# Kernel tuning notes

Hardware: AMD Instinct MI355X
Metric: run time of the kernel (lower is better)

Reference implementation:

```python
import jax, jax.numpy as jnp
import numpy as np

N, E = 50000, 800000
IN, EIN, HID, OUT = 128, 64, 256, 256
L, H = 3, 4
D = HID // H  # per-head out_feats


def setup_inputs() -> dict:
    key = jax.random.key(0)
    ks = jax.random.split(key, 20)
    s = 0.02
    return {
        "h": jax.random.normal(ks[0], (N, IN), jnp.float32),
        "efeat": jax.random.normal(ks[1], (E, EIN), jnp.float32),
        "src": jax.random.randint(ks[2], (E,), 0, N, jnp.int32),
        "dst": jax.random.randint(ks[3], (E,), 0, N, jnp.int32),
        "enc_w": jax.random.normal(ks[4], (IN, HID), jnp.float32) * s,
        "enc_b": jnp.zeros((HID,), jnp.float32),
        "eenc_w": jax.random.normal(ks[5], (EIN, HID), jnp.float32) * s,
        "eenc_b": jnp.zeros((HID,), jnp.float32),
        "Wn": jax.random.normal(ks[6], (L, HID, HID), jnp.float32) * s,
        "We": jax.random.normal(ks[7], (L, HID, HID), jnp.float32) * s,
        "al": jax.random.normal(ks[8], (L, H, D), jnp.float32) * s,
        "ar": jax.random.normal(ks[9], (L, H, D), jnp.float32) * s,
        "ae": jax.random.normal(ks[10], (L, H, D), jnp.float32) * s,
        "ln_g": jnp.ones((L, HID), jnp.float32),
        "ln_b": jnp.zeros((L, HID), jnp.float32),
        "out_w": jax.random.normal(ks[11], (HID, OUT), jnp.float32) * s,
        "out_b": jnp.zeros((OUT,), jnp.float32),
    }


def reference(h, efeat, src, dst, enc_w, enc_b, eenc_w, eenc_b,
              Wn, We, al, ar, ae, ln_g, ln_b, out_w, out_b):
    # Dropout layers act as identity (eval mode).
    n = h.shape[0]
    x = h @ enc_w + enc_b                      # [N, HID] node encoder
    ef = efeat @ eenc_w + eenc_b               # [E, HID] edge encoder
    nl, nh, nd = al.shape
    for l in range(nl):
        res = x
        feat = (x @ Wn[l]).reshape(n, nh, nd)          # [N,H,D]
        eft = (ef @ We[l]).reshape(-1, nh, nd)         # [E,H,D]
        el = jnp.sum(feat * al[l], axis=-1)            # [N,H]
        er = jnp.sum(feat * ar[l], axis=-1)            # [N,H]
        ee = jnp.sum(eft * ae[l], axis=-1)             # [E,H]
        e = jax.nn.leaky_relu(el[src] + er[dst] + ee, 0.2)  # [E,H]
        # edge softmax over incoming edges of each dst node
        m = jax.lax.stop_gradient(jax.ops.segment_max(e, dst, num_segments=n))
        a = jnp.exp(e - m[dst])
        ssum = jax.ops.segment_sum(a, dst, num_segments=n)
        alpha = a / ssum[dst]                          # [E,H]
        agg = jax.ops.segment_sum(alpha[:, :, None] * feat[src], dst,
                                  num_segments=n)      # [N,H,D]
        x = jax.nn.relu(agg.reshape(n, nh * nd))
        y = x + res
        mu = jnp.mean(y, axis=-1, keepdims=True)
        var = jnp.var(y, axis=-1, keepdims=True)
        x = (y - mu) / jnp.sqrt(var + 1e-5) * ln_g[l] + ln_b[l]
    return x @ out_w + out_b
```

## Files before the change

kernel.cpp:

```cpp
#include <hip/hip_runtime.h>
#include <math.h>


typedef __attribute__((ext_vector_type(8))) short bf16x8;
typedef __attribute__((ext_vector_type(8))) unsigned short u16x8;
typedef __attribute__((ext_vector_type(4))) float f32x4;

__device__ __forceinline__ ushort f2b(float f) {
    unsigned u; __builtin_memcpy(&u, &f, 4);
    unsigned r = u + 0x7FFF + ((u >> 16) & 1);
    return (ushort)(r >> 16);
}
__device__ __forceinline__ float b2f(ushort u) {
    unsigned x = (unsigned)u << 16;
    float f; __builtin_memcpy(&f, &x, 4);
    return f;
}

__global__ void k_deg(const int* __restrict__ dst, int* __restrict__ deg, int E) {
    int e = blockIdx.x * 256 + threadIdx.x;
    if (e < E) atomicAdd(&deg[dst[e]], 1);
}

__global__ void k_bsum(const int* __restrict__ deg, int* __restrict__ bsum, int n) {
    __shared__ int wsum[4];
    int tid = threadIdx.x;
    int idx = blockIdx.x * 1024 + tid * 4;
    int4 v = make_int4(0, 0, 0, 0);
    if (idx + 3 < n) v = *(const int4*)(deg + idx);
    else {
        if (idx + 0 < n) v.x = deg[idx + 0];
        if (idx + 1 < n) v.y = deg[idx + 1];
        if (idx + 2 < n) v.z = deg[idx + 2];
    }
    int s = v.x + v.y + v.z + v.w;
#pragma unroll
    for (int off = 32; off; off >>= 1) s += __shfl_down(s, off, 64);
    if ((tid & 63) == 0) wsum[tid >> 6] = s;
    __syncthreads();
    if (tid == 0) bsum[blockIdx.x] = wsum[0] + wsum[1] + wsum[2] + wsum[3];
}

__global__ void k_bscan(const int* __restrict__ bsum, int* __restrict__ boff,
                        int* __restrict__ rowp, int NB, int n) {
    int tid = threadIdx.x;
    int v = (tid < NB) ? bsum[tid] : 0;
    int sc = v;
#pragma unroll
    for (int off = 1; off < 64; off <<= 1) {
        int t = __shfl_up(sc, off, 64);
        if ((tid & 63) >= off) sc += t;
    }
    if (tid < NB) boff[tid] = sc - v;
    if (tid == 63) rowp[n] = sc;
}

__global__ void k_bwrite(const int* __restrict__ deg, const int* __restrict__ boff,
                         int* __restrict__ rowp, int* __restrict__ cursor, int n) {
    __shared__ int wsum[4];
    __shared__ int woff_sh[4];
    int tid = threadIdx.x;
    int lane = tid & 63, wid = tid >> 6;
    int idx = blockIdx.x * 1024 + tid * 4;
    int4 v = make_int4(0, 0, 0, 0);
    if (idx + 3 < n) v = *(const int4*)(deg + idx);
    else {
        if (idx + 0 < n) v.x = deg[idx + 0];
        if (idx + 1 < n) v.y = deg[idx + 1];
        if (idx + 2 < n) v.z = deg[idx + 2];
    }
    int sum4 = v.x + v.y + v.z + v.w;
    int sc = sum4;
#pragma unroll
    for (int off = 1; off < 64; off <<= 1) {
        int t = __shfl_up(sc, off, 64);
        if (lane >= off) sc += t;
    }
    if (lane == 63) wsum[wid] = sc;
    __syncthreads();
    if (tid < 4) {
        int o = 0;
        for (int w = 0; w < tid; w++) o += wsum[w];
        woff_sh[tid] = o;
    }
    __syncthreads();
    int ex = boff[blockIdx.x] + woff_sh[wid] + (sc - sum4);
    int p0 = ex, p1 = ex + v.x, p2 = p1 + v.y, p3 = p2 + v.z;
    if (idx + 0 < n) { rowp[idx + 0] = p0; cursor[idx + 0] = p0; }
    if (idx + 1 < n) { rowp[idx + 1] = p1; cursor[idx + 1] = p1; }
    if (idx + 2 < n) { rowp[idx + 2] = p2; cursor[idx + 2] = p2; }
    if (idx + 3 < n) { rowp[idx + 3] = p3; cursor[idx + 3] = p3; }
}

__global__ void k_scatter(const int* __restrict__ dst, const int* __restrict__ src,
                          int* __restrict__ cursor, int* __restrict__ eid,
                          int* __restrict__ esrc, int E) {
    int e = blockIdx.x * 256 + threadIdx.x;
    if (e < E) {
        int pos = atomicAdd(&cursor[dst[e]], 1);
        eid[pos] = e;
        esrc[pos] = src[e];
    }
}

__global__ void k_ew(const float* __restrict__ We, const float* __restrict__ ae,
                     float* __restrict__ ew) {
    int t = blockIdx.x * 256 + threadIdx.x;
    if (t >= 3072) return;
    int l = t >> 10, r = t & 1023;
    int k = r >> 2, h = r & 3;
    const float* w = We + (size_t)l * 65536 + (size_t)k * 256 + h * 64;
    const float* a = ae + l * 256 + h * 64;
    float s = 0.f;
    for (int d = 0; d < 64; d++) s += w[d] * a[d];
    ew[t] = s;
}

__global__ void k_eew(const float* __restrict__ eenc_w, const float* __restrict__ eenc_b,
                      const float* __restrict__ ew, float* __restrict__ eew2,
                      float* __restrict__ eeb) {
    int t = blockIdx.x * 256 + threadIdx.x;
    if (t < 768) {
        int j = t / 12, lh = t % 12;
        int l = lh >> 2, h = lh & 3;
        float s = 0.f;
        for (int k = 0; k < 256; k++) s += eenc_w[j * 256 + k] * ew[l * 1024 + k * 4 + h];
        eew2[j * 12 + lh] = s;
    } else if (t < 780) {
        int lh = t - 768;
        int l = lh >> 2, h = lh & 3;
        float s = 0.f;
        for (int k = 0; k < 256; k++) s += eenc_b[k] * ew[l * 1024 + k * 4 + h];
        eeb[lh] = s;
    }
}

__global__ __launch_bounds__(256) void k_ee(const float* __restrict__ efeat,
                                            const float* __restrict__ eew2,
                                            const float* __restrict__ eeb,
                                            const int* __restrict__ eid,
                                            float* __restrict__ ee_l,
                                            int E) {
    const int tid = threadIdx.x;
    const int lane = tid & 63;
    const int wave = tid >> 6;
    const int q = lane & 7;
    const int g8 = lane >> 3;

    float W[8][12];
#pragma unroll
    for (int u = 0; u < 4; u++)
#pragma unroll
        for (int t = 0; t < 12; t++) {
            W[u][t]     = eew2[(q * 4 + u) * 12 + t];
            W[u + 4][t] = eew2[(32 + q * 4 + u) * 12 + t];
        }
    float Bv[12];
#pragma unroll
    for (int t = 0; t < 12; t++) Bv[t] = eeb[t];

    const int base = blockIdx.x * 128 + wave * 32;
#pragma unroll
    for (int p = 0; p < 4; p++) {
        int pos = base + p * 8 + g8;
        if (pos >= E) return;
        int e = eid[pos];
        float4 v0 = *(const float4*)(efeat + (size_t)e * 64 + q * 4);
        float4 v1 = *(const float4*)(efeat + (size_t)e * 64 + 32 + q * 4);
        float acc[12];
#pragma unroll
        for (int t = 0; t < 12; t++)
            acc[t] = v0.x * W[0][t] + v0.y * W[1][t] + v0.z * W[2][t] + v0.w * W[3][t] +
                     v1.x * W[4][t] + v1.y * W[5][t] + v1.z * W[6][t] + v1.w * W[7][t];
#pragma unroll
        for (int m = 1; m < 8; m <<= 1)
#pragma unroll
            for (int t = 0; t < 12; t++) acc[t] += __shfl_xor(acc[t], m, 64);
        if (q == 0) {
#pragma unroll
            for (int l = 0; l < 3; l++) {
                float4 o = make_float4(acc[l * 4 + 0] + Bv[l * 4 + 0],
                                       acc[l * 4 + 1] + Bv[l * 4 + 1],
                                       acc[l * 4 + 2] + Bv[l * 4 + 2],
                                       acc[l * 4 + 3] + Bv[l * 4 + 3]);
                *(float4*)(ee_l + (size_t)l * E * 4 + (size_t)pos * 4) = o;
            }
        }
    }
}

__global__ void k_prep(const float* __restrict__ h, const float* __restrict__ enc_w,
                       const float* __restrict__ Wn, const float* __restrict__ out_w,
                       ushort* __restrict__ hb, ushort* __restrict__ encT,
                       ushort* __restrict__ WnT, ushort* __restrict__ outT, int n4) {
    int t = blockIdx.x * 256 + threadIdx.x;
    if (t < n4) {
        float4 v = *(const float4*)(h + (size_t)t * 4);
        ushort4 o;
        o.x = f2b(v.x); o.y = f2b(v.y); o.z = f2b(v.z); o.w = f2b(v.w);
        *(ushort4*)(hb + (size_t)t * 4) = o;
        return;
    }
    t -= n4;
    if (t < 32768) {
        int nn = t >> 7, k = t & 127;
        encT[t] = f2b(enc_w[k * 256 + nn]);
        return;
    }
    t -= 32768;
    if (t < 3 * 65536) {
        int l = t >> 16, r = t & 65535;
        int nn = r >> 8, k = r & 255;
        WnT[(size_t)l * 65536 + r] = f2b(Wn[(size_t)l * 65536 + k * 256 + nn]);
        return;
    }
    t -= 3 * 65536;
    if (t < 65536) {
        int nn = t >> 8, k = t & 255;
        outT[t] = f2b(out_w[k * 256 + nn]);
    }
}

template <int KTILES, bool BIAS, bool STORE_F32, bool STORE_BF16>
__global__ __launch_bounds__(256) void gemm_mfma(const ushort* __restrict__ A,
                                                 const ushort* __restrict__ BT,
                                                 const float* __restrict__ bias,
                                                 float* __restrict__ Cf,
                                                 ushort* __restrict__ Cb, int M) {
    constexpr int K = KTILES * 32;
    __shared__ __align__(16) ushort As[128 * 32];
    __shared__ __align__(16) ushort Bs[128 * 32];
    const int tid = threadIdx.x;
    const int wave = tid >> 6;
    const int lane = tid & 63;
    const int rowBase = blockIdx.x * 128;
    const int colBase = blockIdx.y * 128;
    const int sRow = lane >> 2;
    const int sCol = (lane & 3) * 8;
    const int c0 = wave * 2, c1 = wave * 2 + 1;

    const ushort* gA0 = A + (size_t)(rowBase + c0 * 16 + sRow) * K + sCol;
    const ushort* gA1 = A + (size_t)(rowBase + c1 * 16 + sRow) * K + sCol;
    const ushort* gB0 = BT + (size_t)(colBase + c0 * 16 + sRow) * K + sCol;
    const ushort* gB1 = BT + (size_t)(colBase + c1 * 16 + sRow) * K + sCol;
    ushort* lA0 = As + c0 * 512;
    ushort* lA1 = As + c1 * 512;
    ushort* lB0 = Bs + c0 * 512;
    ushort* lB1 = Bs + c1 * 512;

    f32x4 acc[4][4] = {};
    const int wr = (wave >> 1) * 64, wc = (wave & 1) * 64;
    const int ml = lane & 15, q = lane >> 4;

    for (int kt = 0; kt < KTILES; ++kt) {
        __builtin_amdgcn_global_load_lds(
            (const __attribute__((address_space(1))) unsigned*)(gA0 + kt * 32),
            (__attribute__((address_space(3))) unsigned*)lA0, 16, 0, 0);
        __builtin_amdgcn_global_load_lds(
            (const __attribute__((address_space(1))) unsigned*)(gA1 + kt * 32),
            (__attribute__((address_space(3))) unsigned*)lA1, 16, 0, 0);
        __builtin_amdgcn_global_load_lds(
            (const __attribute__((address_space(1))) unsigned*)(gB0 + kt * 32),
            (__attribute__((address_space(3))) unsigned*)lB0, 16, 0, 0);
        __builtin_amdgcn_global_load_lds(
            (const __attribute__((address_space(1))) unsigned*)(gB1 + kt * 32),
            (__attribute__((address_space(3))) unsigned*)lB1, 16, 0, 0);
        __syncthreads();
        bf16x8 af[4], bfr[4];
#pragma unroll
        for (int i = 0; i < 4; i++)
            af[i] = *(const bf16x8*)&As[(wr + i * 16 + ml) * 32 + q * 8];
#pragma unroll
        for (int j = 0; j < 4; j++)
            bfr[j] = *(const bf16x8*)&Bs[(wc + j * 16 + ml) * 32 + q * 8];
#pragma unroll
        for (int i = 0; i < 4; i++)
#pragma unroll
            for (int j = 0; j < 4; j++)
                acc[i][j] = __builtin_amdgcn_mfma_f32_16x16x32_bf16(af[i], bfr[j], acc[i][j],
                                                                    0, 0, 0);
        __syncthreads();
    }

#pragma unroll
    for (int j = 0; j < 4; j++) {
        const int col = colBase + wc + j * 16 + ml;
        const float bb = BIAS ? bias[col] : 0.f;
#pragma unroll
        for (int i = 0; i < 4; i++) {
#pragma unroll
            for (int r = 0; r < 4; r++) {
                const int row = rowBase + wr + i * 16 + q * 4 + r;
                if (row < M) {
                    float v = acc[i][j][r] + bb;
                    if (STORE_F32) Cf[(size_t)row * 256 + col] = v;
                    if (STORE_BF16) Cb[(size_t)row * 256 + col] = f2b(v);
                }
            }
        }
    }
}

__global__ __launch_bounds__(256) void k_elr(const ushort* __restrict__ feat,
                                             const float* __restrict__ al,
                                             const float* __restrict__ ar,
                                             float* __restrict__ el,
                                             float* __restrict__ er, int N) {
    int lane = threadIdx.x & 63;
    int n = blockIdx.x * 4 + (threadIdx.x >> 6);
    if (n >= N) return;
    ushort4 f4 = *(const ushort4*)&feat[(size_t)n * 256 + lane * 4];
    float4 a4 = *(const float4*)&al[lane * 4];
    float4 r4 = *(const float4*)&ar[lane * 4];
    float f0 = b2f(f4.x), f1 = b2f(f4.y), f2 = b2f(f4.z), f3 = b2f(f4.w);
    float va = f0 * a4.x + f1 * a4.y + f2 * a4.z + f3 * a4.w;
    float vr = f0 * r4.x + f1 * r4.y + f2 * r4.z + f3 * r4.w;
#pragma unroll
    for (int m = 1; m < 16; m <<= 1) {
        va += __shfl_xor(va, m, 64);
        vr += __shfl_xor(vr, m, 64);
    }
    if ((lane & 15) == 0) {
        int h = lane >> 4;
        el[n * 4 + h] = va;
        er[n * 4 + h] = vr;
    }
}

__global__ __launch_bounds__(256) void k_agg(const int* __restrict__ rowp,
                                             const int* __restrict__ esrc,
                                             const float* __restrict__ ee,
                                             const float* __restrict__ el,
                                             const float* __restrict__ er,
                                             const ushort* __restrict__ feat,
                                             ushort* __restrict__ xb,
                                             const float* __restrict__ g,
                                             const float* __restrict__ b, int N) {
    __shared__ float w_sh[4][64][4];
    __shared__ int s_sh[4][64];
    const int wv = threadIdx.x >> 6;
    const int lane = threadIdx.x & 63;
    const int n = blockIdx.x * 4 + wv;
    if (n >= N) return;
    const int start = rowp[n], end = rowp[n + 1];
    const int half = lane >> 5;
    const int c = lane & 31;
    const int h = c >> 3;

    float4 e4 = *(const float4*)(er + (size_t)n * 4);
    float ern[4] = {e4.x, e4.y, e4.z, e4.w};
    float wsum[4] = {0.f, 0.f, 0.f, 0.f};
    float acc[8] = {0.f, 0.f, 0.f, 0.f, 0.f, 0.f, 0.f, 0.f};

    for (int cs = start; cs < end; cs += 64) {
        const int m = min(64, end - cs);
        if (lane < m) {
            int pos = cs + lane;
            int s = esrc[pos];
            s_sh[wv][lane] = s;
            float4 eev = *(const float4*)(ee + (size_t)pos * 4);
            float4 elv = *(const float4*)(el + (size_t)s * 4);
            float ea[4] = {eev.x, eev.y, eev.z, eev.w};
            float la[4] = {elv.x, elv.y, elv.z, elv.w};
#pragma unroll
            for (int hh = 0; hh < 4; hh++) {
                float sc = la[hh] + ern[hh] + ea[hh];
                sc = (sc > 0.f) ? sc : 0.2f * sc;
                float w = __expf(sc);
                w_sh[wv][lane][hh] = w;
                wsum[hh] += w;
            }
        }
        asm volatile("s_waitcnt lgkmcnt(0)" ::: "memory");
        __builtin_amdgcn_sched_barrier(0);
        for (int j = half; j < m; j += 2) {
            int s = s_sh[wv][j];
            float w = w_sh[wv][j][h];
            u16x8 p = *(const u16x8*)&feat[(size_t)s * 256 + c * 8];
#pragma unroll
            for (int u = 0; u < 8; u++) acc[u] += w * b2f((ushort)p[u]);
        }
        asm volatile("s_waitcnt lgkmcnt(0)" ::: "memory");
        __builtin_amdgcn_sched_barrier(0);
    }

#pragma unroll
    for (int u = 0; u < 8; u++) acc[u] += __shfl_xor(acc[u], 32, 64);

#pragma unroll
    for (int mm = 1; mm < 64; mm <<= 1)
#pragma unroll
        for (int hh = 0; hh < 4; hh++) wsum[hh] += __shfl_xor(wsum[hh], mm, 64);

    float inv = (end > start) ? 1.f / wsum[h] : 0.f;
    u16x8 xr = *(const u16x8*)&xb[(size_t)n * 256 + c * 8];
    float y[8];
    float s1 = 0.f, s2 = 0.f;
#pragma unroll
    for (int u = 0; u < 8; u++) {
        float v = fmaxf(acc[u] * inv, 0.f);
        y[u] = v + b2f((ushort)xr[u]);
        s1 += y[u];
        s2 += y[u] * y[u];
    }
#pragma unroll
    for (int mm = 1; mm < 64; mm <<= 1) {
        s1 += __shfl_xor(s1, mm, 64);
        s2 += __shfl_xor(s2, mm, 64);
    }
    float mu = s1 * (1.f / 512.f);
    float var = s2 * (1.f / 512.f) - mu * mu;
    float rstd = rsqrtf(var + 1e-5f);
    float4 gv0 = *(const float4*)&g[c * 8];
    float4 gv1 = *(const float4*)&g[c * 8 + 4];
    float4 bv0 = *(const float4*)&b[c * 8];
    float4 bv1 = *(const float4*)&b[c * 8 + 4];
    float ga[8] = {gv0.x, gv0.y, gv0.z, gv0.w, gv1.x, gv1.y, gv1.z, gv1.w};
    float ba[8] = {bv0.x, bv0.y, bv0.z, bv0.w, bv1.x, bv1.y, bv1.z, bv1.w};
    u16x8 ob;
#pragma unroll
    for (int u = 0; u < 8; u++) ob[u] = f2b((y[u] - mu) * rstd * ga[u] + ba[u]);
    if (half == 0)
        *(u16x8*)&xb[(size_t)n * 256 + c * 8] = ob;
}

extern "C" void kernel_launch(void* const* d_in, const int* in_sizes, int n_in,
                              void* d_out, int out_size, void* d_ws, size_t ws_size,
                              hipStream_t stream) {
    const float* h      = (const float*)d_in[0];
    const float* efeat  = (const float*)d_in[1];
    const int*   src    = (const int*)d_in[2];
    const int*   dst    = (const int*)d_in[3];
    const float* enc_w  = (const float*)d_in[4];
    const float* enc_b  = (const float*)d_in[5];
    const float* eenc_w = (const float*)d_in[6];
    const float* eenc_b = (const float*)d_in[7];
    const float* Wn     = (const float*)d_in[8];
    const float* We     = (const float*)d_in[9];
    const float* al     = (const float*)d_in[10];
    const float* ar     = (const float*)d_in[11];
    const float* ae     = (const float*)d_in[12];
    const float* ln_g   = (const float*)d_in[13];
    const float* ln_b   = (const float*)d_in[14];
    const float* out_w  = (const float*)d_in[15];
    const float* out_b  = (const float*)d_in[16];

    const int N = in_sizes[0] / 128;
    const int E = in_sizes[2];
    const int Mpad = ((N + 127) / 128) * 128;
    const int NB = (N + 1023) / 1024;

    char* ws = (char*)d_ws;
    size_t off = 0;
    auto alloc = [&](size_t bytes) -> char* {
        char* p = ws + off;
        off += (bytes + 255) & ~(size_t)255;
        return p;
    };
    ushort* Xb     = (ushort*)alloc((size_t)Mpad * 256 * 2);
    ushort* F      = (ushort*)alloc((size_t)Mpad * 256 * 2);
    ushort* hb     = (ushort*)alloc((size_t)Mpad * 128 * 2);
    float*  el     = (float*)alloc((size_t)N * 4 * 4);
    float*  er     = (float*)alloc((size_t)N * 4 * 4);
    float*  ee_l   = (float*)alloc((size_t)E * 12 * 4);
    int*    esrc   = (int*)alloc((size_t)E * 4);
    int*    eid    = (int*)alloc((size_t)E * 4);
    int*    deg    = (int*)alloc((size_t)N * 4);
    int*    rowp   = (int*)alloc((size_t)(N + 1) * 4);
    int*    cursor = (int*)alloc((size_t)N * 4);
    int*    bsum   = (int*)alloc(64 * 4);
    int*    boff   = (int*)alloc(64 * 4);
    float*  ew     = (float*)alloc(3072 * 4);
    float*  eew2   = (float*)alloc(768 * 4);
    float*  eeb    = (float*)alloc(64);
    ushort* encT   = (ushort*)alloc(256 * 128 * 2);
    ushort* WnT    = (ushort*)alloc(3 * 256 * 256 * 2);
    ushort* outT   = (ushort*)alloc(256 * 256 * 2);
    (void)ws_size; (void)n_in; (void)out_size;

    hipMemsetAsync(deg, 0, (size_t)N * 4, stream);
    k_deg<<<(E + 255) / 256, 256, 0, stream>>>(dst, deg, E);
    k_bsum<<<NB, 256, 0, stream>>>(deg, bsum, N);
    k_bscan<<<1, 64, 0, stream>>>(bsum, boff, rowp, NB, N);
    k_bwrite<<<NB, 256, 0, stream>>>(deg, boff, rowp, cursor, N);
    k_scatter<<<(E + 255) / 256, 256, 0, stream>>>(dst, src, cursor, eid, esrc, E);

    k_ew<<<12, 256, 0, stream>>>(We, ae, ew);
    k_eew<<<4, 256, 0, stream>>>(eenc_w, eenc_b, ew, eew2, eeb);
    k_ee<<<(E + 127) / 128, 256, 0, stream>>>(efeat, eew2, eeb, eid, ee_l, E);

    const int n4 = N * 128 / 4;
    k_prep<<<(n4 + 32768 + 4 * 65536 + 255) / 256, 256, 0, stream>>>(
        h, enc_w, Wn, out_w, hb, encT, WnT, outT, n4);

    dim3 gG(Mpad / 128, 2);
    gemm_mfma<4, true, false, true><<<gG, 256, 0, stream>>>(hb, encT, enc_b,
                                                            nullptr, Xb, N);

    for (int l = 0; l < 3; l++) {
        gemm_mfma<8, false, false, true><<<gG, 256, 0, stream>>>(
            Xb, WnT + (size_t)l * 65536, nullptr, nullptr, F, N);
        k_elr<<<(N + 3) / 4, 256, 0, stream>>>(F, al + l * 256, ar + l * 256, el, er, N);
        k_agg<<<(N + 3) / 4, 256, 0, stream>>>(rowp, esrc, ee_l + (size_t)l * E * 4,
                                               el, er, F, Xb, ln_g + l * 256,
                                               ln_b + l * 256, N);
    }
    gemm_mfma<8, true, true, false><<<gG, 256, 0, stream>>>(Xb, outT, out_b,
                                                            (float*)d_out, nullptr, N);
}
```

Before: 829.9 us.

## Fuse el/er into GEMM epilogue, store edge scores as bf16, merge prep kernels

```diff
diff --git a/kernel.cpp b/kernel.cpp
--- a/kernel.cpp
+++ b/kernel.cpp
@@ -103,17 +103,49 @@
     }
 }
 
-__global__ void k_ew(const float* __restrict__ We, const float* __restrict__ ae,
-                     float* __restrict__ ew) {
+__global__ void k_prep(const float* __restrict__ h, const float* __restrict__ enc_w,
+                       const float* __restrict__ Wn, const float* __restrict__ out_w,
+                       const float* __restrict__ We, const float* __restrict__ ae,
+                       ushort* __restrict__ hb, ushort* __restrict__ encT,
+                       ushort* __restrict__ WnT, ushort* __restrict__ outT,
+                       float* __restrict__ ew, int n4) {
     int t = blockIdx.x * 256 + threadIdx.x;
-    if (t >= 3072) return;
-    int l = t >> 10, r = t & 1023;
-    int k = r >> 2, h = r & 3;
-    const float* w = We + (size_t)l * 65536 + (size_t)k * 256 + h * 64;
-    const float* a = ae + l * 256 + h * 64;
-    float s = 0.f;
-    for (int d = 0; d < 64; d++) s += w[d] * a[d];
-    ew[t] = s;
+    if (t < n4) {
+        float4 v = *(const float4*)(h + (size_t)t * 4);
+        ushort4 o;
+        o.x = f2b(v.x); o.y = f2b(v.y); o.z = f2b(v.z); o.w = f2b(v.w);
+        *(ushort4*)(hb + (size_t)t * 4) = o;
+        return;
+    }
+    t -= n4;
+    if (t < 32768) {
+        int nn = t >> 7, k = t & 127;
+        encT[t] = f2b(enc_w[k * 256 + nn]);
+        return;
+    }
+    t -= 32768;
+    if (t < 3 * 65536) {
+        int l = t >> 16, r = t & 65535;
+        int nn = r >> 8, k = r & 255;
+        WnT[(size_t)l * 65536 + r] = f2b(Wn[(size_t)l * 65536 + k * 256 + nn]);
+        return;
+    }
+    t -= 3 * 65536;
+    if (t < 65536) {
+        int nn = t >> 8, k = t & 255;
+        outT[t] = f2b(out_w[k * 256 + nn]);
+        return;
+    }
+    t -= 65536;
+    if (t < 3072) {
+        int l = t >> 10, r = t & 1023;
+        int k = r >> 2, hh = r & 3;
+        const float* w = We + (size_t)l * 65536 + (size_t)k * 256 + hh * 64;
+        const float* a = ae + l * 256 + hh * 64;
+        float s = 0.f;
+        for (int d = 0; d < 64; d++) s += w[d] * a[d];
+        ew[t] = s;
+    }
 }
 
 __global__ void k_eew(const float* __restrict__ eenc_w, const float* __restrict__ eenc_b,
@@ -139,7 +171,7 @@
                                             const float* __restrict__ eew2,
                                             const float* __restrict__ eeb,
                                             const int* __restrict__ eid,
-                                            float* __restrict__ ee_l,
+                                            ushort* __restrict__ ee_l,
                                             int E) {
     const int tid = threadIdx.x;
     const int lane = tid & 63;
@@ -160,11 +192,13 @@
     for (int t = 0; t < 12; t++) Bv[t] = eeb[t];
 
     const int base = blockIdx.x * 128 + wave * 32;
+    int my_eid = 0;
+    if (lane < 32 && base + lane < E) my_eid = eid[base + lane];
 #pragma unroll
     for (int p = 0; p < 4; p++) {
         int pos = base + p * 8 + g8;
         if (pos >= E) return;
-        int e = eid[pos];
+        int e = __shfl(my_eid, p * 8 + g8, 64);
         float4 v0 = *(const float4*)(efeat + (size_t)e * 64 + q * 4);
         float4 v1 = *(const float4*)(efeat + (size_t)e * 64 + 32 + q * 4);
         float acc[12];
@@ -179,54 +213,27 @@
         if (q == 0) {
 #pragma unroll
             for (int l = 0; l < 3; l++) {
-                float4 o = make_float4(acc[l * 4 + 0] + Bv[l * 4 + 0],
-                                       acc[l * 4 + 1] + Bv[l * 4 + 1],
-                                       acc[l * 4 + 2] + Bv[l * 4 + 2],
-                                       acc[l * 4 + 3] + Bv[l * 4 + 3]);
-                *(float4*)(ee_l + (size_t)l * E * 4 + (size_t)pos * 4) = o;
+                ushort4 o;
+                o.x = f2b(acc[l * 4 + 0] + Bv[l * 4 + 0]);
+                o.y = f2b(acc[l * 4 + 1] + Bv[l * 4 + 1]);
+                o.z = f2b(acc[l * 4 + 2] + Bv[l * 4 + 2]);
+                o.w = f2b(acc[l * 4 + 3] + Bv[l * 4 + 3]);
+                *(ushort4*)(ee_l + (size_t)l * E * 4 + (size_t)pos * 4) = o;
             }
         }
     }
 }
 
-__global__ void k_prep(const float* __restrict__ h, const float* __restrict__ enc_w,
-                       const float* __restrict__ Wn, const float* __restrict__ out_w,
-                       ushort* __restrict__ hb, ushort* __restrict__ encT,
-                       ushort* __restrict__ WnT, ushort* __restrict__ outT, int n4) {
-    int t = blockIdx.x * 256 + threadIdx.x;
-    if (t < n4) {
-        float4 v = *(const float4*)(h + (size_t)t * 4);
-        ushort4 o;
-        o.x = f2b(v.x); o.y = f2b(v.y); o.z = f2b(v.z); o.w = f2b(v.w);
-        *(ushort4*)(hb + (size_t)t * 4) = o;
-        return;
-    }
-    t -= n4;
-    if (t < 32768) {
-        int nn = t >> 7, k = t & 127;
-        encT[t] = f2b(enc_w[k * 256 + nn]);
-        return;
-    }
-    t -= 32768;
-    if (t < 3 * 65536) {
-        int l = t >> 16, r = t & 65535;
-        int nn = r >> 8, k = r & 255;
-        WnT[(size_t)l * 65536 + r] = f2b(Wn[(size_t)l * 65536 + k * 256 + nn]);
-        return;
-    }
-    t -= 3 * 65536;
-    if (t < 65536) {
-        int nn = t >> 8, k = t & 255;
-        outT[t] = f2b(out_w[k * 256 + nn]);
-    }
-}
-
-template <int KTILES, bool BIAS, bool STORE_F32, bool STORE_BF16>
+template <int KTILES, bool BIAS, bool STORE_F32, bool STORE_BF16, bool ELR>
 __global__ __launch_bounds__(256) void gemm_mfma(const ushort* __restrict__ A,
                                                  const ushort* __restrict__ BT,
                                                  const float* __restrict__ bias,
                                                  float* __restrict__ Cf,
-                                                 ushort* __restrict__ Cb, int M) {
+                                                 ushort* __restrict__ Cb,
+                                                 const float* __restrict__ al,
+                                                 const float* __restrict__ ar,
+                                                 float* __restrict__ el,
+                                                 float* __restrict__ er, int M) {
     constexpr int K = KTILES * 32;
     __shared__ __align__(16) ushort As[128 * 32];
     __shared__ __align__(16) ushort Bs[128 * 32];
@@ -299,37 +306,43 @@
             }
         }
     }
-}
-
-__global__ __launch_bounds__(256) void k_elr(const ushort* __restrict__ feat,
-                                             const float* __restrict__ al,
-                                             const float* __restrict__ ar,
-                                             float* __restrict__ el,
-                                             float* __restrict__ er, int N) {
-    int lane = threadIdx.x & 63;
-    int n = blockIdx.x * 4 + (threadIdx.x >> 6);
-    if (n >= N) return;
-    ushort4 f4 = *(const ushort4*)&feat[(size_t)n * 256 + lane * 4];
-    float4 a4 = *(const float4*)&al[lane * 4];
-    float4 r4 = *(const float4*)&ar[lane * 4];
-    float f0 = b2f(f4.x), f1 = b2f(f4.y), f2 = b2f(f4.z), f3 = b2f(f4.w);
-    float va = f0 * a4.x + f1 * a4.y + f2 * a4.z + f3 * a4.w;
-    float vr = f0 * r4.x + f1 * r4.y + f2 * r4.z + f3 * r4.w;
-#pragma unroll
-    for (int m = 1; m < 16; m <<= 1) {
-        va += __shfl_xor(va, m, 64);
-        vr += __shfl_xor(vr, m, 64);
-    }
-    if ((lane & 15) == 0) {
-        int h = lane >> 4;
-        el[n * 4 + h] = va;
-        er[n * 4 + h] = vr;
+
+    if (ELR) {
+        const int hh = (colBase + wc) >> 6;
+        float alv[4], arv[4];
+#pragma unroll
+        for (int j = 0; j < 4; j++) {
+            alv[j] = al[hh * 64 + j * 16 + ml];
+            arv[j] = ar[hh * 64 + j * 16 + ml];
+        }
+#pragma unroll
+        for (int i = 0; i < 4; i++) {
+#pragma unroll
+            for (int r = 0; r < 4; r++) {
+                float pe = acc[i][0][r] * alv[0] + acc[i][1][r] * alv[1] +
+                           acc[i][2][r] * alv[2] + acc[i][3][r] * alv[3];
+                float pr = acc[i][0][r] * arv[0] + acc[i][1][r] * arv[1] +
+                           acc[i][2][r] * arv[2] + acc[i][3][r] * arv[3];
+#pragma unroll
+                for (int mm = 1; mm < 16; mm <<= 1) {
+                    pe += __shfl_xor(pe, mm, 64);
+                    pr += __shfl_xor(pr, mm, 64);
+                }
+                if (ml == 0) {
+                    const int row = rowBase + wr + i * 16 + q * 4 + r;
+                    if (row < M) {
+                        el[(size_t)row * 4 + hh] = pe;
+                        er[(size_t)row * 4 + hh] = pr;
+                    }
+                }
+            }
+        }
     }
 }
 
 __global__ __launch_bounds__(256) void k_agg(const int* __restrict__ rowp,
                                              const int* __restrict__ esrc,
-                                             const float* __restrict__ ee,
+                                             const ushort* __restrict__ ee,
                                              const float* __restrict__ el,
                                              const float* __restrict__ er,
                                              const ushort* __restrict__ feat,
@@ -358,9 +371,9 @@
             int pos = cs + lane;
             int s = esrc[pos];
             s_sh[wv][lane] = s;
-            float4 eev = *(const float4*)(ee + (size_t)pos * 4);
+            ushort4 eev = *(const ushort4*)(ee + (size_t)pos * 4);
             float4 elv = *(const float4*)(el + (size_t)s * 4);
-            float ea[4] = {eev.x, eev.y, eev.z, eev.w};
+            float ea[4] = {b2f(eev.x), b2f(eev.y), b2f(eev.z), b2f(eev.w)};
             float la[4] = {elv.x, elv.y, elv.z, elv.w};
 #pragma unroll
             for (int hh = 0; hh < 4; hh++) {
@@ -462,7 +475,7 @@
     ushort* hb     = (ushort*)alloc((size_t)Mpad * 128 * 2);
     float*  el     = (float*)alloc((size_t)N * 4 * 4);
     float*  er     = (float*)alloc((size_t)N * 4 * 4);
-    float*  ee_l   = (float*)alloc((size_t)E * 12 * 4);
+    ushort* ee_l   = (ushort*)alloc((size_t)E * 12 * 2);
     int*    esrc   = (int*)alloc((size_t)E * 4);
     int*    eid    = (int*)alloc((size_t)E * 4);
     int*    deg    = (int*)alloc((size_t)N * 4);
@@ -485,26 +498,24 @@
     k_bwrite<<<NB, 256, 0, stream>>>(deg, boff, rowp, cursor, N);
     k_scatter<<<(E + 255) / 256, 256, 0, stream>>>(dst, src, cursor, eid, esrc, E);
 
-    k_ew<<<12, 256, 0, stream>>>(We, ae, ew);
+    const int n4 = N * 128 / 4;
+    k_prep<<<(n4 + 32768 + 4 * 65536 + 3072 + 255) / 256, 256, 0, stream>>>(
+        h, enc_w, Wn, out_w, We, ae, hb, encT, WnT, outT, ew, n4);
     k_eew<<<4, 256, 0, stream>>>(eenc_w, eenc_b, ew, eew2, eeb);
     k_ee<<<(E + 127) / 128, 256, 0, stream>>>(efeat, eew2, eeb, eid, ee_l, E);
 
-    const int n4 = N * 128 / 4;
-    k_prep<<<(n4 + 32768 + 4 * 65536 + 255) / 256, 256, 0, stream>>>(
-        h, enc_w, Wn, out_w, hb, encT, WnT, outT, n4);
-
     dim3 gG(Mpad / 128, 2);
-    gemm_mfma<4, true, false, true><<<gG, 256, 0, stream>>>(hb, encT, enc_b,
-                                                            nullptr, Xb, N);
+    gemm_mfma<4, true, false, true, false><<<gG, 256, 0, stream>>>(
+        hb, encT, enc_b, nullptr, Xb, nullptr, nullptr, nullptr, nullptr, N);
 
     for (int l = 0; l < 3; l++) {
-        gemm_mfma<8, false, false, true><<<gG, 256, 0, stream>>>(
-            Xb, WnT + (size_t)l * 65536, nullptr, nullptr, F, N);
-        k_elr<<<(N + 3) / 4, 256, 0, stream>>>(F, al + l * 256, ar + l * 256, el, er, N);
+        gemm_mfma<8, false, false, true, true><<<gG, 256, 0, stream>>>(
+            Xb, WnT + (size_t)l * 65536, nullptr, nullptr, F,
+            al + l * 256, ar + l * 256, el, er, N);
         k_agg<<<(N + 3) / 4, 256, 0, stream>>>(rowp, esrc, ee_l + (size_t)l * E * 4,
                                                el, er, F, Xb, ln_g + l * 256,
                                                ln_b + l * 256, N);
     }
-    gemm_mfma<8, true, true, false><<<gG, 256, 0, stream>>>(Xb, outT, out_b,
-                                                            (float*)d_out, nullptr, N);
-}
+    gemm_mfma<8, true, true, false, false><<<gG, 256, 0, stream>>>(
+        Xb, outT, out_b, (float*)d_out, nullptr, nullptr, nullptr, nullptr, nullptr, N);
+}
```

After: 811.1 us. 2.3% less time.
